# Kernel tuning notes

Measured on AMD Instinct MI355X. Metric: run time of the kernel, lower is better.

Reference implementation:

```python
import jax, jax.numpy as jnp
import numpy as np

B, S, H = 2, 2048, 1024
NH, NKV, HD = 16, 4, 64

def setup_inputs() -> dict:
    key = jax.random.key(0)
    k1, k2, k3, k4, k5 = jax.random.split(key, 5)
    return {
        "hidden_states": jax.random.normal(k1, (B, S, H), dtype=jnp.float32),
        "attention_mask": jnp.ones((B, S), dtype=jnp.int32),
        "wq": jax.random.normal(k2, (H, NH * HD), dtype=jnp.float32) * 0.02,
        "wk": jax.random.normal(k3, (H, NKV * HD), dtype=jnp.float32) * 0.02,
        "wv": jax.random.normal(k4, (H, NKV * HD), dtype=jnp.float32) * 0.02,
        "wo": jax.random.normal(k5, (NH * HD, 1), dtype=jnp.float32) * 0.02,
    }

def reference(hidden_states, attention_mask, wq, wk, wv, wo):
    bsz, seq_len, _ = hidden_states.shape
    n_rep = NH // NKV
    # projections -> (b, h, s, d)
    q = (hidden_states @ wq).reshape(bsz, seq_len, NH, HD).transpose(0, 2, 1, 3)
    k = (hidden_states @ wk).reshape(bsz, seq_len, NKV, HD).transpose(0, 2, 1, 3)
    v = (hidden_states @ wv).reshape(bsz, seq_len, NKV, HD).transpose(0, 2, 1, 3)
    # repeat_kv == repeat_interleave along head axis
    k = jnp.repeat(k, n_rep, axis=1)
    v = jnp.repeat(v, n_rep, axis=1)
    scores = jnp.einsum('bhqd,bhkd->bhqk', q, k) / np.sqrt(HD).astype(np.float32)
    mask = attention_mask[:, None, None, :]  # (b,1,1,k)
    scores = jnp.where(mask == 0, jnp.float32(-jnp.inf), scores)
    attn = jax.nn.softmax(scores, axis=-1)
    out = jnp.einsum('bhqk,bhkd->bqhd', attn, v).reshape(bsz, seq_len, NH * HD)
    return out @ wo  # (b, s, 1)
```

## Files before the change

### kernel.cpp

```cpp
#include <hip/hip_runtime.h>
#include <stdint.h>


typedef __bf16 bf16x8 __attribute__((ext_vector_type(8)));
typedef float f32x4 __attribute__((ext_vector_type(4)));
typedef float f32x2 __attribute__((ext_vector_type(2)));

__device__ inline unsigned short f2bf(float f) {
    unsigned int u = __builtin_bit_cast(unsigned int, f);
    u += 0x7fff + ((u >> 16) & 1);
    return (unsigned short)(u >> 16);
}
__device__ inline bf16x8 ldfrag(const unsigned short* p) {
    uint4 v = *(const uint4*)p;
    return __builtin_bit_cast(bf16x8, v);
}
__device__ inline void gl2lds16(const void* g, void* l) {
    __builtin_amdgcn_global_load_lds(
        (const __attribute__((address_space(1))) void*)g,
        (__attribute__((address_space(3))) void*)l, 16, 0, 0);
}

#define SCALE_Q 0.18033688011112042f

__global__ __launch_bounds__(256) void prep_kernel(
    const float* __restrict__ wq, const float* __restrict__ wk,
    const float* __restrict__ wv, const float* __restrict__ wo,
    unsigned short* __restrict__ wT)
{
    int bid = blockIdx.x, tid = threadIdx.x;
    if (bid < 320) {
        __shared__ float tile[64 * 65];
        int t = bid;
        int ntile = t / 16, ctile = t % 16;
        int nb = ntile * 64, cb = ctile * 64;
        int tx = tid & 63, ty = tid >> 6;
        for (int i = 0; i < 16; i++) {
            int cl = i * 4 + ty;
            int n = nb + tx;
            float v = (n < 1024) ? wq[(cb + cl) * 1024 + n] * SCALE_Q
                                 : wk[(cb + cl) * 256 + (n - 1024)];
            tile[cl * 65 + tx] = v;
        }
        __syncthreads();
        for (int i = 0; i < 16; i++) {
            int nl = i * 4 + ty;
            wT[(nb + nl) * 1024 + cb + tx] = f2bf(tile[tx * 65 + nl]);
        }
    } else {
        int u = (bid - 320) * 256 + tid;
        int n2 = u >> 10, c = u & 1023;
        if (n2 < 16) {
            int h = n2, kv = h >> 2;
            const float* wvr = wv + c * 256 + kv * 64;
            const float* wor = wo + h * 64;
            float s = 0.f;
            #pragma unroll 8
            for (int d = 0; d < 64; d++) s += wvr[d] * wor[d];
            wT[(1280 + n2) * 1024 + c] = f2bf(s);
        } else {
            wT[(1280 + n2) * 1024 + c] = 0;
        }
    }
}

__global__ __launch_bounds__(256) void gemm_kernel(
    const float* __restrict__ hs, const unsigned short* __restrict__ wT,
    unsigned short* __restrict__ Qp, unsigned short* __restrict__ Kp,
    float* __restrict__ vproj)
{
    __shared__ __align__(16) unsigned short Al[2][128 * 32];
    __shared__ __align__(16) float Blf[2][64 * 32];
    int p = blockIdx.x + 11 * blockIdx.y;
    int xcd = p & 7;
    int j = p >> 3;
    int rt = (xcd << 3) + j / 11;
    int nt = j % 11;
    int tid = threadIdx.x;
    int lane = tid & 63, w = tid >> 6;
    int l15 = lane & 15, quad = lane >> 4;
    int wm = (w >> 1) * 64, wn = (w & 1) * 32;

    f32x4 acc[4][2];
    const f32x4 zero = {0.f, 0.f, 0.f, 0.f};
    for (int i = 0; i < 4; i++) for (int j2 = 0; j2 < 2; j2++) acc[i][j2] = zero;

    int arow = nt * 128, rrow = rt * 64;
    int srowA = w * 32 + (lane >> 2);
    int scolA = (lane & 3) * 8;
    const unsigned short* ga = wT + (size_t)(arow + srowA) * 1024 + scolA;
    int lofsA = (w * 32) * 32;
    int rB = lane >> 3, chB = lane & 7;
    int swzB = chB ^ rB;
    const float* gb = hs + (size_t)(rrow + w * 16 + rB) * 1024 + swzB * 4;
    int lofsB = (w * 16) * 32;

    gl2lds16(ga,             Al[0] + lofsA);
    gl2lds16(ga + 16 * 1024, Al[0] + lofsA + 16 * 32);
    gl2lds16(gb,             Blf[0] + lofsB);
    gl2lds16(gb + 8 * 1024,  Blf[0] + lofsB + 8 * 32);
    ga += 32; gb += 32;
    __syncthreads();

    for (int kk = 0; kk < 32; kk++) {
        int cur = kk & 1, nxt = cur ^ 1;
        if (kk < 31) {
            gl2lds16(ga,             Al[nxt] + lofsA);
            gl2lds16(ga + 16 * 1024, Al[nxt] + lofsA + 16 * 32);
            gl2lds16(gb,             Blf[nxt] + lofsB);
            gl2lds16(gb + 8 * 1024,  Blf[nxt] + lofsB + 8 * 32);
            ga += 32; gb += 32;
        }
        bf16x8 af[4], bfr[2];
        for (int i = 0; i < 4; i++)
            af[i] = ldfrag(Al[cur] + (wm + i * 16 + l15) * 32 + quad * 8);
        for (int j2 = 0; j2 < 2; j2++) {
            int r = wn + j2 * 16 + l15;
            int rx = r & 7;
            const float* rowp = Blf[cur] + r * 32;
            float4 f0 = *(const float4*)(rowp + (((quad * 2)     ^ rx) << 2));
            float4 f1 = *(const float4*)(rowp + (((quad * 2 + 1) ^ rx) << 2));
            bf16x8 bb;
            bb[0] = (__bf16)f0.x; bb[1] = (__bf16)f0.y;
            bb[2] = (__bf16)f0.z; bb[3] = (__bf16)f0.w;
            bb[4] = (__bf16)f1.x; bb[5] = (__bf16)f1.y;
            bb[6] = (__bf16)f1.z; bb[7] = (__bf16)f1.w;
            bfr[j2] = bb;
        }
        for (int i = 0; i < 4; i++)
            for (int j2 = 0; j2 < 2; j2++)
                acc[i][j2] = __builtin_amdgcn_mfma_f32_16x16x32_bf16(af[i], bfr[j2], acc[i][j2], 0, 0, 0);
        __syncthreads();
    }

    for (int i = 0; i < 4; i++) {
        for (int j2 = 0; j2 < 2; j2++) {
            int nw = nt * 128 + wm + i * 16 + quad * 4;
            int r  = rt * 64 + wn + j2 * 16 + l15;
            if (nt < 8) {
                ushort4 o;
                o.x = f2bf(acc[i][j2][0]); o.y = f2bf(acc[i][j2][1]);
                o.z = f2bf(acc[i][j2][2]); o.w = f2bf(acc[i][j2][3]);
                *(ushort4*)(Qp + (size_t)r * 1024 + nw) = o;
            } else if (nt < 10) {
                ushort4 o;
                o.x = f2bf(acc[i][j2][0]); o.y = f2bf(acc[i][j2][1]);
                o.z = f2bf(acc[i][j2][2]); o.w = f2bf(acc[i][j2][3]);
                *(ushort4*)(Kp + (size_t)r * 256 + (nw - 1024)) = o;
            } else {
                for (int rg = 0; rg < 4; rg++) {
                    int h = nw + rg - 1280;
                    if (h < 16)
                        vproj[((size_t)(r >> 11) * 16 + h) * 2048 + (r & 2047)] = acc[i][j2][rg];
                }
            }
        }
    }
}

__global__ __launch_bounds__(256) void attn_kernel(
    const unsigned short* __restrict__ Qp, const unsigned short* __restrict__ Kp,
    const float* __restrict__ vproj, const int* __restrict__ mask,
    float2* __restrict__ part)
{
    __shared__ __align__(16) unsigned short Kl[256 * 64];
    __shared__ __align__(16) float vpml[4 * 256];
    __shared__ __align__(16) float biasl[256];
    int qt = blockIdx.x;
    int b = blockIdx.y >> 2, kv = blockIdx.y & 3;
    int ks = blockIdx.z;
    int tid = threadIdx.x, lane = tid & 63, w = tid >> 6;
    int l15 = lane & 15, quad = lane >> 4;
    int h = kv * 4 + w;
    int k0 = ks * 256;
    int qrow0 = qt * 64;

    {
        int swz = (lane & 7) ^ ((lane >> 3) & 7);
        const unsigned short* kbase =
            Kp + (size_t)(b * 2048 + k0 + w * 64 + (lane >> 3)) * 256 + kv * 64 + swz * 8;
        unsigned short* ldst = Kl + (w * 64) * 64;
        #pragma unroll
        for (int j = 0; j < 8; j++)
            gl2lds16(kbase + (size_t)(j * 8) * 256, ldst + j * 8 * 64);
    }

    bf16x8 qf[4][2];
    for (int qs = 0; qs < 4; qs++) {
        const unsigned short* qp =
            Qp + (size_t)(b * 2048 + qrow0 + qs * 16 + l15) * 1024 + h * 64 + quad * 8;
        qf[qs][0] = ldfrag(qp);
        qf[qs][1] = ldfrag(qp + 32);
    }

    {
        int h2 = tid >> 6, kk = (tid & 63) * 4;
        *(float4*)(vpml + h2 * 256 + kk) =
            *(const float4*)(vproj + ((size_t)b * 16 + kv * 4 + h2) * 2048 + k0 + kk);
    }
    if (tid < 64) {
        int4 mm = *(const int4*)(mask + b * 2048 + k0 + tid * 4);
        float4 bb;
        bb.x = mm.x ? 0.f : -30000.f;
        bb.y = mm.y ? 0.f : -30000.f;
        bb.z = mm.z ? 0.f : -30000.f;
        bb.w = mm.w ? 0.f : -30000.f;
        *(float4*)(biasl + tid * 4) = bb;
    }
    __syncthreads();

    f32x2 nd[4];
    const f32x2 zero2 = {0.f, 0.f};
    for (int qs = 0; qs < 4; qs++) nd[qs] = zero2;

    for (int t8 = 0; t8 < 16; t8++) {
        int r0 = t8 * 16 + l15;
        int rx = r0 & 7;
        bf16x8 a0 = ldfrag(Kl + r0 * 64 + ((quad ^ rx) * 8));
        bf16x8 a1 = ldfrag(Kl + r0 * 64 + (((quad ^ rx) ^ 4) * 8));
        f32x4 vpm4 = *(const f32x4*)(vpml + w * 256 + t8 * 16 + quad * 4);
        f32x4 c4   = *(const f32x4*)(biasl + t8 * 16 + quad * 4);
        for (int qs = 0; qs < 4; qs++) {
            __builtin_amdgcn_s_setprio(1);
            f32x4 d = __builtin_amdgcn_mfma_f32_16x16x32_bf16(a0, qf[qs][0], c4, 0, 0, 0);
            d = __builtin_amdgcn_mfma_f32_16x16x32_bf16(a1, qf[qs][1], d, 0, 0, 0);
            __builtin_amdgcn_s_setprio(0);
            for (int r = 0; r < 4; r++) {
                float e = __builtin_amdgcn_exp2f(d[r]);
                f32x2 m = {vpm4[r], 1.0f};
                nd[qs] += m * e;
            }
        }
    }
    for (int qs = 0; qs < 4; qs++) {
        float n = nd[qs][0], dd = nd[qs][1];
        n += __shfl_xor(n, 16);  n += __shfl_xor(n, 32);
        dd += __shfl_xor(dd, 16); dd += __shfl_xor(dd, 32);
        if (quad == 0) {
            int q = qrow0 + qs * 16 + l15;
            part[((size_t)(b * 2048 + q) * 16 + h) * 8 + ks] = make_float2(n, dd);
        }
    }
}

__global__ __launch_bounds__(256) void combine_kernel(
    const float2* __restrict__ part, float* __restrict__ out)
{
    int wid = (blockIdx.x * 256 + threadIdx.x) >> 6;
    int lane = threadIdx.x & 63;
    const float2* base = part + (size_t)wid * 128;
    float2 p0 = base[lane];
    float2 p1 = base[64 + lane];
    for (int m = 1; m <= 4; m <<= 1) {
        p0.x += __shfl_xor(p0.x, m); p0.y += __shfl_xor(p0.y, m);
        p1.x += __shfl_xor(p1.x, m); p1.y += __shfl_xor(p1.y, m);
    }
    float v = p0.x / p0.y + p1.x / p1.y;
    for (int m = 8; m <= 32; m <<= 1) v += __shfl_xor(v, m);
    if (lane == 0) out[wid] = v;
}

extern "C" void kernel_launch(void* const* d_in, const int* in_sizes, int n_in,
                              void* d_out, int out_size, void* d_ws, size_t ws_size,
                              hipStream_t stream)
{
    const float* hs  = (const float*)d_in[0];
    const int* mask  = (const int*)d_in[1];
    const float* wq  = (const float*)d_in[2];
    const float* wk  = (const float*)d_in[3];
    const float* wv  = (const float*)d_in[4];
    const float* wo  = (const float*)d_in[5];

    char* ws = (char*)d_ws;
    unsigned short* wT = (unsigned short*)ws;
    unsigned short* Qp = (unsigned short*)(ws + 2883584);
    unsigned short* Kp = (unsigned short*)(ws + 11272192);
    float* vproj       = (float*)(ws + 13369344);
    float2* part       = (float2*)(ws + 13631488);

    prep_kernel<<<832, 256, 0, stream>>>(wq, wk, wv, wo, wT);
    gemm_kernel<<<dim3(11, 64), 256, 0, stream>>>(hs, wT, Qp, Kp, vproj);
    attn_kernel<<<dim3(32, 8, 8), 256, 0, stream>>>(Qp, Kp, vproj, mask, part);
    combine_kernel<<<1024, 256, 0, stream>>>(part, (float*)d_out);
}
```

Baseline: 138.9 us.

## Triple-buffer GEMM LDS loads with explicit vmcnt waits

```diff
diff --git a/kernel.cpp b/kernel.cpp
--- a/kernel.cpp
+++ b/kernel.cpp
@@ -69,8 +69,8 @@
     unsigned short* __restrict__ Qp, unsigned short* __restrict__ Kp,
     float* __restrict__ vproj)
 {
-    __shared__ __align__(16) unsigned short Al[2][128 * 32];
-    __shared__ __align__(16) float Blf[2][64 * 32];
+    __shared__ __align__(16) unsigned short Al[3][128 * 32];
+    __shared__ __align__(16) float Blf[3][64 * 32];
     int p = blockIdx.x + 11 * blockIdx.y;
     int xcd = p & 7;
     int j = p >> 3;
@@ -95,43 +95,51 @@
     const float* gb = hs + (size_t)(rrow + w * 16 + rB) * 1024 + swzB * 4;
     int lofsB = (w * 16) * 32;
 
-    gl2lds16(ga,             Al[0] + lofsA);
-    gl2lds16(ga + 16 * 1024, Al[0] + lofsA + 16 * 32);
-    gl2lds16(gb,             Blf[0] + lofsB);
-    gl2lds16(gb + 8 * 1024,  Blf[0] + lofsB + 8 * 32);
+#define GEMM_STAGE(SB) \
+    gl2lds16(ga,             Al[SB] + lofsA); \
+    gl2lds16(ga + 16 * 1024, Al[SB] + lofsA + 16 * 32); \
+    gl2lds16(gb,             Blf[SB] + lofsB); \
+    gl2lds16(gb + 8 * 1024,  Blf[SB] + lofsB + 8 * 32); \
     ga += 32; gb += 32;
-    __syncthreads();
-
-    for (int kk = 0; kk < 32; kk++) {
-        int cur = kk & 1, nxt = cur ^ 1;
-        if (kk < 31) {
-            gl2lds16(ga,             Al[nxt] + lofsA);
-            gl2lds16(ga + 16 * 1024, Al[nxt] + lofsA + 16 * 32);
-            gl2lds16(gb,             Blf[nxt] + lofsB);
-            gl2lds16(gb + 8 * 1024,  Blf[nxt] + lofsB + 8 * 32);
-            ga += 32; gb += 32;
-        }
-        bf16x8 af[4], bfr[2];
-        for (int i = 0; i < 4; i++)
-            af[i] = ldfrag(Al[cur] + (wm + i * 16 + l15) * 32 + quad * 8);
-        for (int j2 = 0; j2 < 2; j2++) {
-            int r = wn + j2 * 16 + l15;
-            int rx = r & 7;
-            const float* rowp = Blf[cur] + r * 32;
-            float4 f0 = *(const float4*)(rowp + (((quad * 2)     ^ rx) << 2));
-            float4 f1 = *(const float4*)(rowp + (((quad * 2 + 1) ^ rx) << 2));
-            bf16x8 bb;
-            bb[0] = (__bf16)f0.x; bb[1] = (__bf16)f0.y;
-            bb[2] = (__bf16)f0.z; bb[3] = (__bf16)f0.w;
-            bb[4] = (__bf16)f1.x; bb[5] = (__bf16)f1.y;
-            bb[6] = (__bf16)f1.z; bb[7] = (__bf16)f1.w;
-            bfr[j2] = bb;
-        }
-        for (int i = 0; i < 4; i++)
-            for (int j2 = 0; j2 < 2; j2++)
-                acc[i][j2] = __builtin_amdgcn_mfma_f32_16x16x32_bf16(af[i], bfr[j2], acc[i][j2], 0, 0, 0);
-        __syncthreads();
-    }
+
+#define GEMM_COMPUTE(CB) { \
+    bf16x8 af[4], bfr[2]; \
+    for (int i = 0; i < 4; i++) \
+        af[i] = ldfrag(Al[CB] + (wm + i * 16 + l15) * 32 + quad * 8); \
+    for (int j2 = 0; j2 < 2; j2++) { \
+        int r = wn + j2 * 16 + l15; \
+        int rx = r & 7; \
+        const float* rowp = Blf[CB] + r * 32; \
+        float4 f0 = *(const float4*)(rowp + (((quad * 2)     ^ rx) << 2)); \
+        float4 f1 = *(const float4*)(rowp + (((quad * 2 + 1) ^ rx) << 2)); \
+        bf16x8 bb; \
+        bb[0] = (__bf16)f0.x; bb[1] = (__bf16)f0.y; \
+        bb[2] = (__bf16)f0.z; bb[3] = (__bf16)f0.w; \
+        bb[4] = (__bf16)f1.x; bb[5] = (__bf16)f1.y; \
+        bb[6] = (__bf16)f1.z; bb[7] = (__bf16)f1.w; \
+        bfr[j2] = bb; \
+    } \
+    for (int i = 0; i < 4; i++) \
+        for (int j2 = 0; j2 < 2; j2++) \
+            acc[i][j2] = __builtin_amdgcn_mfma_f32_16x16x32_bf16(af[i], bfr[j2], acc[i][j2], 0, 0, 0); }
+
+#define WAITB(N) \
+    asm volatile("s_waitcnt vmcnt(" #N ")" ::: "memory"); \
+    __builtin_amdgcn_s_barrier();
+
+    GEMM_STAGE(0)
+    GEMM_STAGE(1)
+    for (int kt = 0; kt < 10; kt++) {
+        GEMM_STAGE(2) WAITB(8) GEMM_COMPUTE(0) __builtin_amdgcn_s_barrier();
+        GEMM_STAGE(0) WAITB(8) GEMM_COMPUTE(1) __builtin_amdgcn_s_barrier();
+        GEMM_STAGE(1) WAITB(8) GEMM_COMPUTE(2) __builtin_amdgcn_s_barrier();
+    }
+    WAITB(4) GEMM_COMPUTE(0)
+    WAITB(0) GEMM_COMPUTE(1)
+
+#undef GEMM_STAGE
+#undef GEMM_COMPUTE
+#undef WAITB
 
     for (int i = 0; i < 4; i++) {
         for (int j2 = 0; j2 < 2; j2++) {
```

Result: faster. 136.0 us (-2.1%).
